# Performance work log

Hardware: AMD Instinct MI355X
Metric: run time of the kernel (lower is better)

The kernel has to match this reference:

```python
import jax, jax.numpy as jnp
import numpy as np

SPATIAL_SHAPES = np.array([[100, 100], [50, 50], [25, 25], [13, 13]], dtype=np.int32)
EMBED, NH, NL, NP = 256, 8, 4, 4
HD = EMBED // NH  # 32


def setup_inputs() -> dict:
    key = jax.random.key(0)
    ks = jax.random.split(key, 12)
    bs, nq = 4, 4000
    nv = int((SPATIAL_SHAPES[:, 0] * SPATIAL_SHAPES[:, 1]).sum())  # 13294
    s_lin = 1.0 / np.sqrt(EMBED)  # xavier-ish scale
    s_small = 0.02                # offsets/weights heads start near init
    return {
        "query": jax.random.normal(ks[0], (bs, nq, EMBED), jnp.float32),
        "value": jax.random.normal(ks[1], (bs, nv, EMBED), jnp.float32),
        "reference_points": jax.random.uniform(ks[2], (bs, nq, NL, 2), jnp.float32),
        "spatial_shapes": jnp.asarray(SPATIAL_SHAPES),
        "W_off": jax.random.normal(ks[3], (EMBED, NH * NL * NP * 2), jnp.float32) * s_small,
        "b_off": jax.random.normal(ks[4], (NH * NL * NP * 2,), jnp.float32) * s_small,
        "W_attn": jax.random.normal(ks[5], (EMBED, NH * NL * NP), jnp.float32) * s_small,
        "b_attn": jax.random.normal(ks[6], (NH * NL * NP,), jnp.float32) * s_small,
        "W_val": jax.random.normal(ks[7], (EMBED, EMBED), jnp.float32) * s_lin,
        "b_val": jnp.zeros((EMBED,), jnp.float32),
        "W_out": jax.random.normal(ks[8], (EMBED, EMBED), jnp.float32) * s_lin,
        "b_out": jnp.zeros((EMBED,), jnp.float32),
    }


def _bilinear_sample(val_l, H, W, x, y):
    """grid_sample(mode=bilinear, padding=zeros, align_corners=False) equivalent.
    val_l: [bs, nh, H*W, hd]; x, y: [bs, nh, nq, np] pixel-space coords.
    Returns [bs, nh, nq, np, hd]."""
    x0 = jnp.floor(x)
    y0 = jnp.floor(y)
    bs, nh, nq, npts = x.shape
    out = 0.0
    for dx, dy in ((0, 0), (1, 0), (0, 1), (1, 1)):
        xi = x0 + dx
        yi = y0 + dy
        w = (1.0 - jnp.abs(x - xi)) * (1.0 - jnp.abs(y - yi))
        valid = (xi >= 0) & (xi < W) & (yi >= 0) & (yi < H)
        idx = (jnp.clip(yi, 0, H - 1) * W + jnp.clip(xi, 0, W - 1)).astype(jnp.int32)
        g = jnp.take_along_axis(val_l, idx.reshape(bs, nh, nq * npts, 1), axis=2)
        g = g.reshape(bs, nh, nq, npts, -1)
        out = out + g * (w * valid.astype(w.dtype))[..., None]
    return out


def reference(query, value, reference_points, spatial_shapes,
              W_off, b_off, W_attn, b_attn, W_val, b_val, W_out, b_out):
    shapes = np.asarray(spatial_shapes)  # static level shapes
    bs, nq, _ = query.shape
    # value projection -> per-head layout [bs, nh, nv, hd]
    v = (value @ W_val + b_val).reshape(bs, -1, NH, HD).transpose(0, 2, 1, 3)
    # sampling offsets and attention weights from query
    off = (query @ W_off + b_off).reshape(bs, nq, NH, NL, NP, 2)
    attn = jax.nn.softmax((query @ W_attn + b_attn).reshape(bs, nq, NH, NL * NP), axis=-1)
    attn = attn.reshape(bs, nq, NH, NL, NP)
    # normalized sampling locations; normalizer = (W, H) per level
    normalizer = jnp.asarray(np.stack([shapes[:, 1], shapes[:, 0]], -1), jnp.float32)
    loc = reference_points[:, :, None, :, None, :] + off / normalizer[None, None, None, :, None, :]
    out = jnp.zeros((bs, NH, nq, HD), query.dtype)
    start = 0
    for l in range(NL):
        H, W = int(shapes[l, 0]), int(shapes[l, 1])
        val_l = v[:, :, start:start + H * W, :]
        # pixel coords with align_corners=False: p = loc*size - 0.5
        x = loc[:, :, :, l, :, 0].transpose(0, 2, 1, 3) * W - 0.5  # [bs,nh,nq,np]
        y = loc[:, :, :, l, :, 1].transpose(0, 2, 1, 3) * H - 0.5
        sampled = _bilinear_sample(val_l, H, W, x, y)  # [bs,nh,nq,np,hd]
        out = out + jnp.einsum('bhqpd,bqhp->bhqd', sampled, attn[:, :, :, l, :])
        start += H * W
    out = out.transpose(0, 2, 1, 3).reshape(bs, nq, EMBED)
    return out @ W_out + b_out
```

## Files before the change

### kernel.cpp

```cpp
#include <hip/hip_runtime.h>
#include <hip/hip_bf16.h>

#define EMBED 256
#define NH 8
#define NL 4
#define NP 4
#define HD 32
#define BS 4
#define NQ 4000
#define NV 13294

using f32x4   = __attribute__((ext_vector_type(4))) float;
using bf16x8  = __attribute__((ext_vector_type(8))) short;

__device__ __forceinline__ float bf2f_lo(unsigned u) {
    union { unsigned u; float f; } x; x.u = u << 16; return x.f;
}
__device__ __forceinline__ float bf2f_hi(unsigned u) {
    union { unsigned u; float f; } x; x.u = u & 0xffff0000u; return x.f;
}
__device__ __forceinline__ unsigned short f2bf(float f) {
    union { float f; unsigned u; } x; x.f = f;
    unsigned u = x.u;
    return (unsigned short)((u + 0x7fffu + ((u >> 16) & 1u)) >> 16);
}
__device__ __forceinline__ unsigned cvtpk(float lo, float hi) {
    unsigned r;
    asm("v_cvt_pk_bf16_f32 %0, %1, %2" : "=v"(r) : "v"(lo), "v"(hi));
    return r;
}

__device__ __forceinline__ void async16(const void* g, void* l) {
    __builtin_amdgcn_global_load_lds(
        (const __attribute__((address_space(1))) void*)g,
        (__attribute__((address_space(3))) void*)l, 16, 0, 0);
}

template<int N> __device__ __forceinline__ void wait_vmcnt() {
    if constexpr (N == 0)      asm volatile("s_waitcnt vmcnt(0)" ::: "memory");
    else if constexpr (N == 2) asm volatile("s_waitcnt vmcnt(2)" ::: "memory");
    else if constexpr (N == 3) asm volatile("s_waitcnt vmcnt(3)" ::: "memory");
}

__device__ __forceinline__ int xcd_chunk(int s, int nwg) {
    const int q = nwg >> 3, r = nwg & 7;
    const int x = s & 7, i = s >> 3;
    return (x < r ? x * (q + 1) : r * (q + 1) + (x - r) * q) + i;
}

__global__ __launch_bounds__(256) void msda_prep_k(
    const float* __restrict__ W_val, const float* __restrict__ W_out,
    const float* __restrict__ W_off, const float* __restrict__ W_attn,
    const float* __restrict__ b_off, const float* __restrict__ b_attn,
    unsigned short* __restrict__ Wt_val, unsigned short* __restrict__ Wt_out,
    unsigned short* __restrict__ Wt_qa, float* __restrict__ b_qa)
{
    int i = blockIdx.x * 256 + threadIdx.x;
    if (i < 384) b_qa[i] = (i < 256) ? b_off[i] : b_attn[i - 256];
    if (i < 65536) {
        int r = i >> 8, c = i & 255;
        Wt_val[c * 256 + r] = f2bf(W_val[i]);
    } else if (i < 131072) {
        int j = i - 65536, r = j >> 8, c = j & 255;
        Wt_out[c * 256 + r] = f2bf(W_out[j]);
    } else if (i < 229376) {
        int j = i - 131072;
        int n = j >> 8, k = j & 255;
        float v = (n < 256) ? W_off[k * 256 + n] : W_attn[k * 128 + (n - 256)];
        Wt_qa[j] = f2bf(v);
    }
}

template<int EPI, bool ABF16>
__device__ __forceinline__ void gemm_body(
    char* lds,
    const void* __restrict__ Ap,
    const unsigned short* __restrict__ Bt,
    const float* __restrict__ bias,
    void* __restrict__ out,
    int M, int N, int mblk, int nblk)
{
    constexpr int K = 256, C = 8;
    constexpr int NI = 2;
    constexpr int ABYTES = 128 * 32 * 2;
    constexpr int BUFB   = ABYTES + 128 * 32 * 2;
    constexpr int LOPS   = ABF16 ? 1 : 2;

    const int m0 = mblk * 128, n0 = nblk * 128;
    const int tid  = threadIdx.x;
    const int w    = tid >> 6;
    const int lane = tid & 63;
    const int quad = lane >> 4;
    const int l16  = lane & 15;
    const int wm   = (w & 1) * 64;
    const int wn   = (w >> 1) * 32;

    const int ar  = tid >> 2;
    const int arg = min(m0 + ar, M - 1);
    const int ak  = (tid & 3) * 8;
    const float*          afp = (const float*)Ap          + (size_t)arg * K + ak;
    const unsigned short* abp = (const unsigned short*)Ap + (size_t)arg * K + ak;

    const char* bgp = (const char*)(Bt + (size_t)(n0 + w * 16 + (lane >> 2)) * K)
                      + (lane & 3) * 16;

    auto issueB = [&](int c, int kb) {
        async16(bgp + c * 64, lds + kb * BUFB + ABYTES + w * 1024);
    };

    float4 aLoR[2], aHiR[2];
    bf16x8 aRegR[2];
    auto loadA = [&](int c) {
        const int p = c & 1;
        if constexpr (ABF16) {
            aRegR[p] = *(const bf16x8*)(abp + c * 32);
        } else {
            aLoR[p] = *(const float4*)(afp + c * 32);
            aHiR[p] = *(const float4*)(afp + c * 32 + 4);
        }
    };
    auto writeA = [&](int c) {
        const int p = c & 1;
        unsigned short* dst = (unsigned short*)(lds + (c % 3) * BUFB) + ar * 32 + ak;
        if constexpr (ABF16) {
            *(bf16x8*)dst = aRegR[p];
        } else {
            union { unsigned u[4]; bf16x8 v; } t;
            t.u[0] = cvtpk(aLoR[p].x, aLoR[p].y); t.u[1] = cvtpk(aLoR[p].z, aLoR[p].w);
            t.u[2] = cvtpk(aHiR[p].x, aHiR[p].y); t.u[3] = cvtpk(aHiR[p].z, aHiR[p].w);
            *(bf16x8*)dst = t.v;
        }
    };

    f32x4 acc[4][NI];
#pragma unroll
    for (int a = 0; a < 4; a++)
#pragma unroll
        for (int b = 0; b < NI; b++) acc[a][b] = (f32x4){0.f, 0.f, 0.f, 0.f};

    loadA(0); issueB(0, 0); loadA(1); issueB(1, 1);
    writeA(0);

#pragma unroll
    for (int c = 0; c < C; c++) {
        if (c < C - 1) wait_vmcnt<LOPS + 1>(); else wait_vmcnt<0>();
        asm volatile("s_waitcnt lgkmcnt(0)" ::: "memory");
        __builtin_amdgcn_s_barrier();
        __builtin_amdgcn_sched_barrier(0);
        if (c + 2 < C) { loadA(c + 2); issueB(c + 2, (c + 2) % 3); }

        const char* aL = lds + (c % 3) * BUFB;
        const char* bL = aL + ABYTES;
        bf16x8 af[4], bfr[NI];
#pragma unroll
        for (int mi = 0; mi < 4; mi++)
            af[mi] = *(const bf16x8*)(aL + (wm + mi * 16 + l16) * 64 + quad * 16);
#pragma unroll
        for (int ni = 0; ni < NI; ni++)
            bfr[ni] = *(const bf16x8*)(bL + (wn + ni * 16 + l16) * 64 + quad * 16);

        if (c + 1 < C) writeA(c + 1);

#pragma unroll
        for (int mi = 0; mi < 4; mi++)
#pragma unroll
            for (int ni = 0; ni < NI; ni++)
                acc[mi][ni] = __builtin_amdgcn_mfma_f32_16x16x32_bf16(af[mi], bfr[ni], acc[mi][ni], 0, 0, 0);
    }

    if constexpr (EPI == 0) {
        __syncthreads();
        unsigned short* cs = (unsigned short*)lds;
#pragma unroll
        for (int ni = 0; ni < NI; ni++) {
            int cl = wn + ni * 16 + l16;
            float bvv = bias[n0 + cl];
#pragma unroll
            for (int mi = 0; mi < 4; mi++)
#pragma unroll
                for (int r = 0; r < 4; r++) {
                    int ml = wm + mi * 16 + quad * 4 + r;
                    cs[ml * 136 + cl] = f2bf(acc[mi][ni][r] + bvv);
                }
        }
        __syncthreads();
        const int seg = tid >> 7, rr = tid & 127;
        const int m = m0 + rr;
        if (m < M) {
            const int b   = m / NV;
            const int pix = m - b * NV;
            const int h   = (n0 >> 5) + seg;
            char* dst = (char*)out + (((size_t)b * 8 + h) * NV + pix) * 64;
            const uint4* s = (const uint4*)&cs[rr * 136 + seg * 32];
#pragma unroll
            for (int j = 0; j < 4; j++) ((uint4*)dst)[j] = s[j];
        }
    } else {
#pragma unroll
        for (int ni = 0; ni < NI; ni++) {
            int cc = n0 + wn + ni * 16 + l16;
            float bvv = bias[cc];
#pragma unroll
            for (int mi = 0; mi < 4; mi++)
#pragma unroll
                for (int r = 0; r < 4; r++) {
                    int m = m0 + wm + mi * 16 + quad * 4 + r;
                    if (m >= M) continue;
                    ((float*)out)[(size_t)m * N + cc] = acc[mi][ni][r] + bvv;
                }
        }
    }
}

__global__ __launch_bounds__(512) void msda_gemm_vq_k(
    const float* __restrict__ value, const float* __restrict__ query,
    const unsigned short* __restrict__ Wt_val, const unsigned short* __restrict__ Wt_qa,
    const float* __restrict__ b_val, const float* __restrict__ b_qa,
    unsigned short* __restrict__ v_buf, float* __restrict__ oa_buf)
{
    extern __shared__ char lds[];
    const int bx = xcd_chunk(blockIdx.x, 832 + 375);
    if (bx < 832) {
        gemm_body<0, false>(lds, value, Wt_val, b_val, v_buf,
                            BS * NV, 256, bx >> 1, bx & 1);
    } else {
        const int j = bx - 832;
        const int mb = j / 3;
        gemm_body<1, false>(lds, query, Wt_qa, b_qa, oa_buf,
                            BS * NQ, 384, mb, j - mb * 3);
    }
}

__global__ __launch_bounds__(256) void msda_gemm_out_k(
    const unsigned short* __restrict__ t_buf,
    const unsigned short* __restrict__ Wt_out,
    const float* __restrict__ b_out,
    float* __restrict__ out)
{
    extern __shared__ char lds[];
    constexpr int K = 256, C = 8, M = BS * NQ, N = 256;
    constexpr int ABYTES = 64 * 32 * 2;
    constexpr int BUFB   = ABYTES + 64 * 32 * 2;
    const int bx = blockIdx.x;
    const int m0 = (bx >> 2) * 64, n0 = (bx & 3) * 64;
    const int tid  = threadIdx.x;
    const int w    = tid >> 6;
    const int lane = tid & 63;
    const int quad = lane >> 4;
    const int l16  = lane & 15;
    const int wn   = w * 16;

    const int ar  = tid >> 2;
    const int ak  = (tid & 3) * 8;
    const unsigned short* abp = t_buf + (size_t)(m0 + ar) * K + ak;

    const char* bgp = (const char*)(Wt_out + (size_t)(n0 + w * 16 + (lane >> 2)) * K)
                      + (lane & 3) * 16;
    auto issueB = [&](int c, int kb) {
        async16(bgp + c * 64, lds + kb * BUFB + ABYTES + w * 1024);
    };

    bf16x8 aRegR[2];
    auto loadA  = [&](int c) { aRegR[c & 1] = *(const bf16x8*)(abp + c * 32); };
    auto writeA = [&](int c) {
        *(bf16x8*)((unsigned short*)(lds + (c % 3) * BUFB) + ar * 32 + ak) = aRegR[c & 1];
    };

    f32x4 acc[4];
#pragma unroll
    for (int a = 0; a < 4; a++) acc[a] = (f32x4){0.f, 0.f, 0.f, 0.f};

    loadA(0); issueB(0, 0); loadA(1); issueB(1, 1);
    writeA(0);

#pragma unroll
    for (int c = 0; c < C; c++) {
        if (c < C - 1) wait_vmcnt<2>(); else wait_vmcnt<0>();
        asm volatile("s_waitcnt lgkmcnt(0)" ::: "memory");
        __builtin_amdgcn_s_barrier();
        __builtin_amdgcn_sched_barrier(0);
        if (c + 2 < C) { loadA(c + 2); issueB(c + 2, (c + 2) % 3); }

        const char* aL = lds + (c % 3) * BUFB;
        const char* bL = aL + ABYTES;
        bf16x8 af[4], bfr;
#pragma unroll
        for (int mi = 0; mi < 4; mi++)
            af[mi] = *(const bf16x8*)(aL + (mi * 16 + l16) * 64 + quad * 16);
        bfr = *(const bf16x8*)(bL + (wn + l16) * 64 + quad * 16);

        if (c + 1 < C) writeA(c + 1);

#pragma unroll
        for (int mi = 0; mi < 4; mi++)
            acc[mi] = __builtin_amdgcn_mfma_f32_16x16x32_bf16(af[mi], bfr, acc[mi], 0, 0, 0);
    }

    const int cc = n0 + wn + l16;
    const float bvv = b_out[cc];
#pragma unroll
    for (int mi = 0; mi < 4; mi++)
#pragma unroll
        for (int r = 0; r < 4; r++) {
            int m = m0 + mi * 16 + quad * 4 + r;
            out[(size_t)m * N + cc] = acc[mi][r] + bvv;
        }
}

__global__ __launch_bounds__(256) void msda_sampler_k(
    const float* __restrict__ refpts,
    const float* __restrict__ oa_buf,
    const unsigned short* __restrict__ v_buf,
    unsigned short* __restrict__ t_out)
{
    __shared__ float  oa_s[4][384];
    __shared__ float  ref_s[4][8];
    __shared__ float4 wtab[528];
    __shared__ int2   itab[528];

    const int tid = threadIdx.x;
    const int q0  = blockIdx.x * 4;

    {
        const float4* src = (const float4*)(oa_buf + (size_t)q0 * 384);
        float4* dst = (float4*)&oa_s[0][0];
        dst[tid] = src[tid];
        if (tid < 128) dst[256 + tid] = src[256 + tid];
        if (tid < 32) ((float*)ref_s)[tid] = refpts[q0 * 8 + tid];
    }
    __syncthreads();

    const int HWs[4]    = {100, 50, 25, 13};
    const int starts[4] = {0, 10000, 12500, 13125};
#pragma unroll
    for (int it = 0; it < 2; it++) {
        int s  = tid + it * 256;
        int i  = s & 15;
        int h  = (s >> 4) & 7;
        int ql = s >> 7;
        int l  = i >> 2, p = i & 3;
        float logit = oa_s[ql][256 + h * 16 + i];
        float m = logit;
#pragma unroll
        for (int off = 1; off < 16; off <<= 1) m = fmaxf(m, __shfl_xor(m, off, 64));
        float e = __expf(logit - m);
        float sum = e;
#pragma unroll
        for (int off = 1; off < 16; off <<= 1) sum += __shfl_xor(sum, off, 64);
        float a = e / sum;

        int Wl = HWs[l];
        float fW = (float)Wl;
        float rx = ref_s[ql][l * 2], ry = ref_s[ql][l * 2 + 1];
        float offx = oa_s[ql][h * 32 + l * 8 + p * 2];
        float offy = oa_s[ql][h * 32 + l * 8 + p * 2 + 1];
        float x = rx * fW + offx - 0.5f;
        float y = ry * fW + offy - 0.5f;
        float xf = floorf(x), yf = floorf(y);
        float fx = x - xf, fy = y - yf;
        int x0 = (int)xf, y0 = (int)yf;
        int x1 = x0 + 1, y1 = y0 + 1;
        float wx0 = (x0 >= 0 && x0 < Wl) ? (1.f - fx) : 0.f;
        float wx1 = (x1 >= 0 && x1 < Wl) ? fx : 0.f;
        float wy0 = (y0 >= 0 && y0 < Wl) ? (1.f - fy) : 0.f;
        float wy1 = (y1 >= 0 && y1 < Wl) ? fy : 0.f;
        int x0c = min(max(x0, 0), Wl - 1), x1c = min(max(x1, 0), Wl - 1);
        int y0c = min(max(y0, 0), Wl - 1), y1c = min(max(y1, 0), Wl - 1);
        int r0 = starts[l] + y0c * Wl, r1 = starts[l] + y1c * Wl;

        int xb = min(max(x0, 0), Wl - 2);
        float wlo = ((x0c == xb)     ? wx0 : 0.f) + ((x1c == xb)     ? wx1 : 0.f);
        float whi = ((x0c == xb + 1) ? wx0 : 0.f) + ((x1c == xb + 1) ? wx1 : 0.f);

        int ti = i * 33 + ql * 8 + h;
        wtab[ti] = make_float4(wy0 * a, wy1 * a, wlo, whi);
        itab[ti] = make_int2(r0 + xb, r1 + xb);
    }
    __syncthreads();

    const int dg4 = tid & 3, xc = (tid >> 2) & 1, h = (tid >> 3) & 7, ql = tid >> 6;
    const int q = q0 + ql;
    const int b = q / NQ;
    const char* base = (const char*)v_buf + ((size_t)(b * 8 + h)) * NV * 64 + dg4 * 16;
    const int tbase = ql * 8 + h;

    float a0 = 0.f, a1 = 0.f, a2 = 0.f, a3 = 0.f;
    float a4 = 0.f, a5 = 0.f, a6 = 0.f, a7 = 0.f;
#pragma unroll
    for (int lp = 0; lp < 16; lp++) {
        float4 wv = wtab[lp * 33 + tbase];
        int2   iv = itab[lp * 33 + tbase];
        uint4 s0 = *(const uint4*)(base + ((unsigned)(iv.x + xc) << 6));
        uint4 s1 = *(const uint4*)(base + ((unsigned)(iv.y + xc) << 6));
        float wx = xc ? wv.w : wv.z;
        float w0 = wx * wv.x, w1 = wx * wv.y;
        a0 += w0 * bf2f_lo(s0.x); a1 += w0 * bf2f_hi(s0.x);
        a2 += w0 * bf2f_lo(s0.y); a3 += w0 * bf2f_hi(s0.y);
        a4 += w0 * bf2f_lo(s0.z); a5 += w0 * bf2f_hi(s0.z);
        a6 += w0 * bf2f_lo(s0.w); a7 += w0 * bf2f_hi(s0.w);
        a0 += w1 * bf2f_lo(s1.x); a1 += w1 * bf2f_hi(s1.x);
        a2 += w1 * bf2f_lo(s1.y); a3 += w1 * bf2f_hi(s1.y);
        a4 += w1 * bf2f_lo(s1.z); a5 += w1 * bf2f_hi(s1.z);
        a6 += w1 * bf2f_lo(s1.w); a7 += w1 * bf2f_hi(s1.w);
    }
    a0 += __shfl_xor(a0, 4, 64); a1 += __shfl_xor(a1, 4, 64);
    a2 += __shfl_xor(a2, 4, 64); a3 += __shfl_xor(a3, 4, 64);
    a4 += __shfl_xor(a4, 4, 64); a5 += __shfl_xor(a5, 4, 64);
    a6 += __shfl_xor(a6, 4, 64); a7 += __shfl_xor(a7, 4, 64);
    if (xc == 0) {
        uint4 o;
        o.x = (unsigned)f2bf(a0) | ((unsigned)f2bf(a1) << 16);
        o.y = (unsigned)f2bf(a2) | ((unsigned)f2bf(a3) << 16);
        o.z = (unsigned)f2bf(a4) | ((unsigned)f2bf(a5) << 16);
        o.w = (unsigned)f2bf(a6) | ((unsigned)f2bf(a7) << 16);
        *(uint4*)(t_out + (size_t)q * 256 + h * 32 + dg4 * 8) = o;
    }
}

extern "C" void kernel_launch(void* const* d_in, const int* in_sizes, int n_in,
                              void* d_out, int out_size, void* d_ws, size_t ws_size,
                              hipStream_t stream) {
    const float* query  = (const float*)d_in[0];
    const float* value  = (const float*)d_in[1];
    const float* refpts = (const float*)d_in[2];
    const float* W_off  = (const float*)d_in[4];
    const float* b_off  = (const float*)d_in[5];
    const float* W_attn = (const float*)d_in[6];
    const float* b_attn = (const float*)d_in[7];
    const float* W_val  = (const float*)d_in[8];
    const float* b_val  = (const float*)d_in[9];
    const float* W_out  = (const float*)d_in[10];
    const float* b_out  = (const float*)d_in[11];

    char* wsp = (char*)d_ws;
    size_t o = 0;
    auto carve = [&](size_t bytes) -> void* {
        void* p = wsp + o; o += (bytes + 255) & ~(size_t)255; return p;
    };
    unsigned short* Wt_val = (unsigned short*)carve(256 * 256 * 2);
    unsigned short* Wt_out = (unsigned short*)carve(256 * 256 * 2);
    unsigned short* Wt_qa  = (unsigned short*)carve(384 * 256 * 2);
    float*          b_qa   = (float*)carve(384 * 4);
    unsigned short* v_buf  = (unsigned short*)carve((size_t)BS * NH * NV * 32 * 2);
    float*          oa_buf = (float*)carve((size_t)BS * NQ * 384 * 4);
    unsigned short* t_buf  = (unsigned short*)carve((size_t)BS * NQ * EMBED * 2);

    msda_prep_k<<<896, 256, 0, stream>>>(W_val, W_out, W_off, W_attn,
                                         b_off, b_attn, Wt_val, Wt_out, Wt_qa, b_qa);

    msda_gemm_vq_k<<<832 + 375, 512, 49152, stream>>>(value, query, Wt_val, Wt_qa,
                                                      b_val, b_qa, v_buf, oa_buf);
    msda_sampler_k<<<(BS * NQ) / 4, 256, 0, stream>>>(refpts, oa_buf, v_buf, t_buf);
    msda_gemm_out_k<<<1000, 256, 24576, stream>>>(t_buf, Wt_out, b_out, (float*)d_out);
}
```

Baseline: 200.4 us.

## Halve queries per sampler block and split bilinear rows across threads; drop XCD remap

The sampler now handles 2 queries per 256-thread block instead of 4. Each thread gathers a single bilinear corner (one y-row and one x-column) rather than two rows, and partial sums are combined with an extra xor-shuffle. This doubles the grid and the thread-level parallelism available to hide gather latency, at the cost of more shuffles and redundant per-block setup. The XCD-aware block remapping in the fused value/query GEMM is also removed, and the output GEMM kernel is moved lower in the file without changes.

```diff
diff --git a/kernel.cpp b/kernel.cpp
--- a/kernel.cpp
+++ b/kernel.cpp
@@ -40,12 +40,6 @@
     if constexpr (N == 0)      asm volatile("s_waitcnt vmcnt(0)" ::: "memory");
     else if constexpr (N == 2) asm volatile("s_waitcnt vmcnt(2)" ::: "memory");
     else if constexpr (N == 3) asm volatile("s_waitcnt vmcnt(3)" ::: "memory");
-}
-
-__device__ __forceinline__ int xcd_chunk(int s, int nwg) {
-    const int q = nwg >> 3, r = nwg & 7;
-    const int x = s & 7, i = s >> 3;
-    return (x < r ? x * (q + 1) : r * (q + 1) + (x - r) * q) + i;
 }
 
 __global__ __launch_bounds__(256) void msda_prep_k(
@@ -219,7 +213,7 @@
     unsigned short* __restrict__ v_buf, float* __restrict__ oa_buf)
 {
     extern __shared__ char lds[];
-    const int bx = xcd_chunk(blockIdx.x, 832 + 375);
+    const int bx = blockIdx.x;
     if (bx < 832) {
         gemm_body<0, false>(lds, value, Wt_val, b_val, v_buf,
                             BS * NV, 256, bx >> 1, bx & 1);
@@ -231,113 +225,33 @@
     }
 }
 
-__global__ __launch_bounds__(256) void msda_gemm_out_k(
-    const unsigned short* __restrict__ t_buf,
-    const unsigned short* __restrict__ Wt_out,
-    const float* __restrict__ b_out,
-    float* __restrict__ out)
-{
-    extern __shared__ char lds[];
-    constexpr int K = 256, C = 8, M = BS * NQ, N = 256;
-    constexpr int ABYTES = 64 * 32 * 2;
-    constexpr int BUFB   = ABYTES + 64 * 32 * 2;
-    const int bx = blockIdx.x;
-    const int m0 = (bx >> 2) * 64, n0 = (bx & 3) * 64;
-    const int tid  = threadIdx.x;
-    const int w    = tid >> 6;
-    const int lane = tid & 63;
-    const int quad = lane >> 4;
-    const int l16  = lane & 15;
-    const int wn   = w * 16;
-
-    const int ar  = tid >> 2;
-    const int ak  = (tid & 3) * 8;
-    const unsigned short* abp = t_buf + (size_t)(m0 + ar) * K + ak;
-
-    const char* bgp = (const char*)(Wt_out + (size_t)(n0 + w * 16 + (lane >> 2)) * K)
-                      + (lane & 3) * 16;
-    auto issueB = [&](int c, int kb) {
-        async16(bgp + c * 64, lds + kb * BUFB + ABYTES + w * 1024);
-    };
-
-    bf16x8 aRegR[2];
-    auto loadA  = [&](int c) { aRegR[c & 1] = *(const bf16x8*)(abp + c * 32); };
-    auto writeA = [&](int c) {
-        *(bf16x8*)((unsigned short*)(lds + (c % 3) * BUFB) + ar * 32 + ak) = aRegR[c & 1];
-    };
-
-    f32x4 acc[4];
-#pragma unroll
-    for (int a = 0; a < 4; a++) acc[a] = (f32x4){0.f, 0.f, 0.f, 0.f};
-
-    loadA(0); issueB(0, 0); loadA(1); issueB(1, 1);
-    writeA(0);
-
-#pragma unroll
-    for (int c = 0; c < C; c++) {
-        if (c < C - 1) wait_vmcnt<2>(); else wait_vmcnt<0>();
-        asm volatile("s_waitcnt lgkmcnt(0)" ::: "memory");
-        __builtin_amdgcn_s_barrier();
-        __builtin_amdgcn_sched_barrier(0);
-        if (c + 2 < C) { loadA(c + 2); issueB(c + 2, (c + 2) % 3); }
-
-        const char* aL = lds + (c % 3) * BUFB;
-        const char* bL = aL + ABYTES;
-        bf16x8 af[4], bfr;
-#pragma unroll
-        for (int mi = 0; mi < 4; mi++)
-            af[mi] = *(const bf16x8*)(aL + (mi * 16 + l16) * 64 + quad * 16);
-        bfr = *(const bf16x8*)(bL + (wn + l16) * 64 + quad * 16);
-
-        if (c + 1 < C) writeA(c + 1);
-
-#pragma unroll
-        for (int mi = 0; mi < 4; mi++)
-            acc[mi] = __builtin_amdgcn_mfma_f32_16x16x32_bf16(af[mi], bfr, acc[mi], 0, 0, 0);
-    }
-
-    const int cc = n0 + wn + l16;
-    const float bvv = b_out[cc];
-#pragma unroll
-    for (int mi = 0; mi < 4; mi++)
-#pragma unroll
-        for (int r = 0; r < 4; r++) {
-            int m = m0 + mi * 16 + quad * 4 + r;
-            out[(size_t)m * N + cc] = acc[mi][r] + bvv;
-        }
-}
-
 __global__ __launch_bounds__(256) void msda_sampler_k(
     const float* __restrict__ refpts,
     const float* __restrict__ oa_buf,
     const unsigned short* __restrict__ v_buf,
     unsigned short* __restrict__ t_out)
 {
-    __shared__ float  oa_s[4][384];
-    __shared__ float  ref_s[4][8];
-    __shared__ float4 wtab[528];
-    __shared__ int2   itab[528];
+    __shared__ float  oa_s[2][384];
+    __shared__ float  ref_s[2][8];
+    __shared__ float4 wtab[272];
+    __shared__ int2   itab[272];
 
     const int tid = threadIdx.x;
-    const int q0  = blockIdx.x * 4;
+    const int q0  = blockIdx.x * 2;
 
     {
         const float4* src = (const float4*)(oa_buf + (size_t)q0 * 384);
-        float4* dst = (float4*)&oa_s[0][0];
-        dst[tid] = src[tid];
-        if (tid < 128) dst[256 + tid] = src[256 + tid];
-        if (tid < 32) ((float*)ref_s)[tid] = refpts[q0 * 8 + tid];
+        if (tid < 192) ((float4*)&oa_s[0][0])[tid] = src[tid];
+        if (tid < 16) ((float*)ref_s)[tid] = refpts[q0 * 8 + tid];
     }
     __syncthreads();
 
     const int HWs[4]    = {100, 50, 25, 13};
     const int starts[4] = {0, 10000, 12500, 13125};
-#pragma unroll
-    for (int it = 0; it < 2; it++) {
-        int s  = tid + it * 256;
-        int i  = s & 15;
-        int h  = (s >> 4) & 7;
-        int ql = s >> 7;
+    {
+        int i  = tid & 15;
+        int h  = (tid >> 4) & 7;
+        int ql = tid >> 7;
         int l  = i >> 2, p = i & 3;
         float logit = oa_s[ql][256 + h * 16 + i];
         float m = logit;
@@ -372,13 +286,14 @@
         float wlo = ((x0c == xb)     ? wx0 : 0.f) + ((x1c == xb)     ? wx1 : 0.f);
         float whi = ((x0c == xb + 1) ? wx0 : 0.f) + ((x1c == xb + 1) ? wx1 : 0.f);
 
-        int ti = i * 33 + ql * 8 + h;
+        int ti = i * 17 + ql * 8 + h;
         wtab[ti] = make_float4(wy0 * a, wy1 * a, wlo, whi);
         itab[ti] = make_int2(r0 + xb, r1 + xb);
     }
     __syncthreads();
 
-    const int dg4 = tid & 3, xc = (tid >> 2) & 1, h = (tid >> 3) & 7, ql = tid >> 6;
+    const int dg4 = tid & 3, xc = (tid >> 2) & 1, yc = (tid >> 3) & 1;
+    const int h = (tid >> 4) & 7, ql = tid >> 7;
     const int q = q0 + ql;
     const int b = q / NQ;
     const char* base = (const char*)v_buf + ((size_t)(b * 8 + h)) * NV * 64 + dg4 * 16;
@@ -388,26 +303,25 @@
     float a4 = 0.f, a5 = 0.f, a6 = 0.f, a7 = 0.f;
 #pragma unroll
     for (int lp = 0; lp < 16; lp++) {
-        float4 wv = wtab[lp * 33 + tbase];
-        int2   iv = itab[lp * 33 + tbase];
-        uint4 s0 = *(const uint4*)(base + ((unsigned)(iv.x + xc) << 6));
-        uint4 s1 = *(const uint4*)(base + ((unsigned)(iv.y + xc) << 6));
-        float wx = xc ? wv.w : wv.z;
-        float w0 = wx * wv.x, w1 = wx * wv.y;
-        a0 += w0 * bf2f_lo(s0.x); a1 += w0 * bf2f_hi(s0.x);
-        a2 += w0 * bf2f_lo(s0.y); a3 += w0 * bf2f_hi(s0.y);
-        a4 += w0 * bf2f_lo(s0.z); a5 += w0 * bf2f_hi(s0.z);
-        a6 += w0 * bf2f_lo(s0.w); a7 += w0 * bf2f_hi(s0.w);
-        a0 += w1 * bf2f_lo(s1.x); a1 += w1 * bf2f_hi(s1.x);
-        a2 += w1 * bf2f_lo(s1.y); a3 += w1 * bf2f_hi(s1.y);
-        a4 += w1 * bf2f_lo(s1.z); a5 += w1 * bf2f_hi(s1.z);
-        a6 += w1 * bf2f_lo(s1.w); a7 += w1 * bf2f_hi(s1.w);
-    }
+        float4 wv = wtab[lp * 17 + tbase];
+        int2   iv = itab[lp * 17 + tbase];
+        int row  = (yc ? iv.y : iv.x) + xc;
+        float w  = (yc ? wv.y : wv.x) * (xc ? wv.w : wv.z);
+        uint4 s = *(const uint4*)(base + ((unsigned)row << 6));
+        a0 += w * bf2f_lo(s.x); a1 += w * bf2f_hi(s.x);
+        a2 += w * bf2f_lo(s.y); a3 += w * bf2f_hi(s.y);
+        a4 += w * bf2f_lo(s.z); a5 += w * bf2f_hi(s.z);
+        a6 += w * bf2f_lo(s.w); a7 += w * bf2f_hi(s.w);
+    }
+    a0 += __shfl_xor(a0, 8, 64); a1 += __shfl_xor(a1, 8, 64);
+    a2 += __shfl_xor(a2, 8, 64); a3 += __shfl_xor(a3, 8, 64);
+    a4 += __shfl_xor(a4, 8, 64); a5 += __shfl_xor(a5, 8, 64);
+    a6 += __shfl_xor(a6, 8, 64); a7 += __shfl_xor(a7, 8, 64);
     a0 += __shfl_xor(a0, 4, 64); a1 += __shfl_xor(a1, 4, 64);
     a2 += __shfl_xor(a2, 4, 64); a3 += __shfl_xor(a3, 4, 64);
     a4 += __shfl_xor(a4, 4, 64); a5 += __shfl_xor(a5, 4, 64);
     a6 += __shfl_xor(a6, 4, 64); a7 += __shfl_xor(a7, 4, 64);
-    if (xc == 0) {
+    if ((tid & 12) == 0) {
         uint4 o;
         o.x = (unsigned)f2bf(a0) | ((unsigned)f2bf(a1) << 16);
         o.y = (unsigned)f2bf(a2) | ((unsigned)f2bf(a3) << 16);
@@ -415,6 +329,82 @@
         o.w = (unsigned)f2bf(a6) | ((unsigned)f2bf(a7) << 16);
         *(uint4*)(t_out + (size_t)q * 256 + h * 32 + dg4 * 8) = o;
     }
+}
+
+__global__ __launch_bounds__(256) void msda_gemm_out_k(
+    const unsigned short* __restrict__ t_buf,
+    const unsigned short* __restrict__ Wt_out,
+    const float* __restrict__ b_out,
+    float* __restrict__ out)
+{
+    extern __shared__ char lds[];
+    constexpr int K = 256, C = 8, N = 256;
+    constexpr int ABYTES = 64 * 32 * 2;
+    constexpr int BUFB   = ABYTES + 64 * 32 * 2;
+    const int bx = blockIdx.x;
+    const int m0 = (bx >> 2) * 64, n0 = (bx & 3) * 64;
+    const int tid  = threadIdx.x;
+    const int w    = tid >> 6;
+    const int lane = tid & 63;
+    const int quad = lane >> 4;
+    const int l16  = lane & 15;
+    const int wn   = w * 16;
+
+    const int ar  = tid >> 2;
+    const int ak  = (tid & 3) * 8;
+    const unsigned short* abp = t_buf + (size_t)(m0 + ar) * K + ak;
+
+    const char* bgp = (const char*)(Wt_out + (size_t)(n0 + w * 16 + (lane >> 2)) * K)
+                      + (lane & 3) * 16;
+    auto issueB = [&](int c, int kb) {
+        async16(bgp + c * 64, lds + kb * BUFB + ABYTES + w * 1024);
+    };
+
+    bf16x8 aRegR[2];
+    auto loadA  = [&](int c) { aRegR[c & 1] = *(const bf16x8*)(abp + c * 32); };
+    auto writeA = [&](int c) {
+        *(bf16x8*)((unsigned short*)(lds + (c % 3) * BUFB) + ar * 32 + ak) = aRegR[c & 1];
+    };
+
+    f32x4 acc[4];
+#pragma unroll
+    for (int a = 0; a < 4; a++) acc[a] = (f32x4){0.f, 0.f, 0.f, 0.f};
+
+    loadA(0); issueB(0, 0); loadA(1); issueB(1, 1);
+    writeA(0);
+
+#pragma unroll
+    for (int c = 0; c < C; c++) {
+        if (c < C - 1) wait_vmcnt<2>(); else wait_vmcnt<0>();
+        asm volatile("s_waitcnt lgkmcnt(0)" ::: "memory");
+        __builtin_amdgcn_s_barrier();
+        __builtin_amdgcn_sched_barrier(0);
+        if (c + 2 < C) { loadA(c + 2); issueB(c + 2, (c + 2) % 3); }
+
+        const char* aL = lds + (c % 3) * BUFB;
+        const char* bL = aL + ABYTES;
+        bf16x8 af[4], bfr;
+#pragma unroll
+        for (int mi = 0; mi < 4; mi++)
+            af[mi] = *(const bf16x8*)(aL + (mi * 16 + l16) * 64 + quad * 16);
+        bfr = *(const bf16x8*)(bL + (wn + l16) * 64 + quad * 16);
+
+        if (c + 1 < C) writeA(c + 1);
+
+#pragma unroll
+        for (int mi = 0; mi < 4; mi++)
+            acc[mi] = __builtin_amdgcn_mfma_f32_16x16x32_bf16(af[mi], bfr, acc[mi], 0, 0, 0);
+    }
+
+    const int cc = n0 + wn + l16;
+    const float bvv = b_out[cc];
+#pragma unroll
+    for (int mi = 0; mi < 4; mi++)
+#pragma unroll
+        for (int r = 0; r < 4; r++) {
+            int m = m0 + mi * 16 + quad * 4 + r;
+            out[(size_t)m * N + cc] = acc[mi][r] + bvv;
+        }
 }
 
 extern "C" void kernel_launch(void* const* d_in, const int* in_sizes, int n_in,
@@ -450,6 +440,6 @@
 
     msda_gemm_vq_k<<<832 + 375, 512, 49152, stream>>>(value, query, Wt_val, Wt_qa,
                                                       b_val, b_qa, v_buf, oa_buf);
-    msda_sampler_k<<<(BS * NQ) / 4, 256, 0, stream>>>(refpts, oa_buf, v_buf, t_buf);
+    msda_sampler_k<<<(BS * NQ) / 2, 256, 0, stream>>>(refpts, oa_buf, v_buf, t_buf);
     msda_gemm_out_k<<<1000, 256, 24576, stream>>>(t_buf, Wt_out, b_out, (float*)d_out);
 }
```

New measurement: 188.7 us. -5.9%, faster.
